# Kernel optimization log

Hardware: AMD Instinct MI355X
Metric: run time of the kernel (lower is better)

Reference implementation:

```python
import jax, jax.numpy as jnp
import numpy as np

NUM_CLASSES = 10
OUT_DIM = 16
NUM_ROUTING = 3
ROUTING_BIAS = 0.1


def _squash(s):
    # s: [B, C, D]; norm over last (out_capsule) dim, matches torch norm(dim=2)
    norm = jnp.linalg.norm(s, axis=2, keepdims=True)
    # s / (1+norm^2) / norm * norm^2 == s * norm / (1 + norm^2)
    return s * norm / (1.0 + norm * norm)


def setup_inputs() -> dict:
    key = jax.random.key(0)
    k1, k2 = jax.random.split(key)
    B, N, IN_DIM = 256, 2304, 8
    x = jax.random.normal(k1, (B, N, IN_DIM), dtype=jnp.float32)
    # kaiming-normal-ish init for W [N, in_dim, classes*out_dim]
    W = jax.random.normal(k2, (N, IN_DIM, NUM_CLASSES * OUT_DIM), dtype=jnp.float32) * np.sqrt(2.0 / IN_DIM)
    return {"x": x, "W": W}


def reference(x, W):
    B, N, _ = x.shape
    # broadcast-multiply+sum in original == per-capsule matmul
    u_hat = jnp.einsum('bni,nio->bno', x, W).reshape(B, N, NUM_CLASSES, OUT_DIM)
    u_hat_sg = jax.lax.stop_gradient(u_hat)
    b = jnp.zeros((B, N, NUM_CLASSES), dtype=x.dtype)
    v = None
    for i in range(NUM_ROUTING):
        c = jax.nn.softmax(b, axis=2)  # [B, N, C]
        if i == NUM_ROUTING - 1:
            s = jnp.einsum('bnc,bncd->bcd', c, u_hat) + ROUTING_BIAS
            v = _squash(s)
        else:
            s = jnp.einsum('bnc,bncd->bcd', c, u_hat_sg) + ROUTING_BIAS
            # NOTE: original updates b with pre-squash s (not v) -- kept faithful
            b = b + jnp.einsum('bncd,bcd->bnc', u_hat_sg, s)
    return v
```

## Files before the change

### kernel.cpp

```cpp
#include <hip/hip_runtime.h>
#include <math.h>

#define B_TOT   256
#define N_TOT   2304
#define IN_DIM  8
#define NC      10
#define OD      16
#define CD      160
#define RBIAS   0.1f

#define BTILE    64
#define NS       192
#define NPB      (N_TOT / NS)
#define NTHREADS 640
#define XR       (NPB * IN_DIM + 4)
#define LB       72
#define NF4      (B_TOT * CD / 4)
#define RCOLS    32
#define RGRPS    8
#define RYPER    (NS / RGRPS)

template <int FIRST>
__global__ __launch_bounds__(NTHREADS) void routing_round(
    const float* __restrict__ x,
    const float* __restrict__ W,
    const float* __restrict__ S_acc,
    float* __restrict__ part)
{
    __shared__ float sh_x[BTILE * XR];
    __shared__ float sh_lg[2][NC * LB];

    const int tid = threadIdx.x;
    const int b0  = blockIdx.x * BTILE;
    const int n0  = blockIdx.y * NPB;
    const int b   = tid & 63;
    const int cu  = __builtin_amdgcn_readfirstlane(tid >> 6);

    {
        const int XT4 = BTILE * (NPB * IN_DIM / 4);
        for (int k = tid; k < XT4; k += NTHREADS) {
            int bb   = k / (NPB * 2);
            int off4 = k - bb * (NPB * 2);
            float4 v = *(const float4*)(x + ((size_t)(b0 + bb) * N_TOT + n0) * IN_DIM + off4 * 4);
            *(float4*)(&sh_x[bb * XR + off4 * 4]) = v;
        }
    }

    float S[OD];
    if (!FIRST) {
        const float4* sp = (const float4*)(S_acc + (size_t)(b0 + b) * CD + cu * OD);
        #pragma unroll
        for (int q = 0; q < 4; q++) ((float4*)S)[q] = sp[q];
    }

    float acc[OD];
    #pragma unroll
    for (int d = 0; d < OD; d++) acc[d] = 0.f;

    __syncthreads();

    const float* Wc = W + cu * OD;

    for (int nn = 0; nn < NPB; nn++) {
        float xf[IN_DIM];
        {
            const float4* xp = (const float4*)(&sh_x[b * XR + nn * IN_DIM]);
            ((float4*)xf)[0] = xp[0];
            ((float4*)xf)[1] = xp[1];
        }

        const float* Wn = Wc + (size_t)(n0 + nn) * (IN_DIM * CD);
        float u[OD];
        #pragma unroll
        for (int d = 0; d < OD; d++) u[d] = xf[0] * Wn[d];
        #pragma unroll
        for (int i = 1; i < IN_DIM; i++) {
            const float* Wi = Wn + i * CD;
            #pragma unroll
            for (int d = 0; d < OD; d++) u[d] = fmaf(xf[i], Wi[d], u[d]);
        }

        if (!FIRST) {
            const int cur = nn & 1;
            float lg = 0.f;
            #pragma unroll
            for (int d = 0; d < OD; d++) lg = fmaf(u[d], S[d], lg);
            sh_lg[cur][cu * LB + b] = lg;
            __syncthreads();

            float m = -1e30f;
            float row[NC];
            #pragma unroll
            for (int k = 0; k < NC; k++) {
                row[k] = sh_lg[cur][k * LB + b];
                m = fmaxf(m, row[k]);
            }
            float den = 0.f;
            #pragma unroll
            for (int k = 0; k < NC; k++) den += __expf(row[k] - m);
            float cw = __expf(lg - m) / den;

            #pragma unroll
            for (int d = 0; d < OD; d++) acc[d] = fmaf(cw, u[d], acc[d]);
        } else {
            #pragma unroll
            for (int d = 0; d < OD; d++) acc[d] += u[d];
        }
    }

    float* dst = part + ((size_t)blockIdx.y * B_TOT + (b0 + b)) * CD + cu * OD;
    #pragma unroll
    for (int q = 0; q < 4; q++)
        ((float4*)dst)[q] = ((float4*)acc)[q];
}

__global__ __launch_bounds__(256) void reduce_round(
    const float* __restrict__ part,
    float* __restrict__ S_acc,
    float* __restrict__ v_out,
    float scale, int round)
{
    __shared__ float4 sh[RGRPS][RCOLS];

    const int col = threadIdx.x & (RCOLS - 1);
    const int grp = threadIdx.x >> 5;
    const int g   = blockIdx.x * RCOLS + col;

    const float4* p4 = (const float4*)part + (size_t)grp * NF4 + g;
    float4 s = { 0.f, 0.f, 0.f, 0.f };
    #pragma unroll 4
    for (int y = 0; y < RYPER; y++) {
        float4 t = p4[(size_t)y * RGRPS * NF4];
        s.x += t.x; s.y += t.y; s.z += t.z; s.w += t.w;
    }
    sh[grp][col] = s;
    __syncthreads();

    if (threadIdx.x < RCOLS) {
        float4 t = { 0.f, 0.f, 0.f, 0.f };
        #pragma unroll
        for (int k = 0; k < RGRPS; k++) {
            float4 q = sh[k][col];
            t.x += q.x; t.y += q.y; t.z += q.z; t.w += q.w;
        }
        t.x = t.x * scale + RBIAS;
        t.y = t.y * scale + RBIAS;
        t.z = t.z * scale + RBIAS;
        t.w = t.w * scale + RBIAS;

        if (round == 0) {
            ((float4*)S_acc)[g] = t;
        } else if (round == 1) {
            float4 o = ((float4*)S_acc)[g];
            o.x += t.x; o.y += t.y; o.z += t.z; o.w += t.w;
            ((float4*)S_acc)[g] = o;
        } else {
            float ss = t.x * t.x + t.y * t.y + t.z * t.z + t.w * t.w;
            ss += __shfl_xor(ss, 1, 64);
            ss += __shfl_xor(ss, 2, 64);
            float norm = sqrtf(ss);
            float k2 = norm / (1.0f + ss);
            float4 v = { t.x * k2, t.y * k2, t.z * k2, t.w * k2 };
            ((float4*)v_out)[g] = v;
        }
    }
}

extern "C" void kernel_launch(void* const* d_in, const int* in_sizes, int n_in,
                              void* d_out, int out_size, void* d_ws, size_t ws_size,
                              hipStream_t stream) {
    const float* x = (const float*)d_in[0];
    const float* W = (const float*)d_in[1];
    float* out = (float*)d_out;

    float* part  = (float*)d_ws;
    float* S_acc = part + (size_t)NS * B_TOT * CD;

    const dim3 rgrid(B_TOT / BTILE, NS);
    const int  RG = NF4 / RCOLS;

    routing_round<1><<<rgrid, NTHREADS, 0, stream>>>(x, W, S_acc, part);
    reduce_round<<<RG, 256, 0, stream>>>(part, S_acc, out, 0.1f, 0);

    routing_round<0><<<rgrid, NTHREADS, 0, stream>>>(x, W, S_acc, part);
    reduce_round<<<RG, 256, 0, stream>>>(part, S_acc, out, 1.0f, 1);

    routing_round<0><<<rgrid, NTHREADS, 0, stream>>>(x, W, S_acc, part);
    reduce_round<<<RG, 256, 0, stream>>>(part, S_acc, out, 1.0f, 2);
}
```

Baseline: 212.4 us.

## Cache u_hat in fp16 workspace for later routing rounds instead of recomputing

The first routing pass now also writes the per-capsule prediction vectors u_hat to workspace in half precision. The two later routing passes read them back instead of recomputing x·W. A software-prefetch of the next capsule's data is added in the cached kernel. The path runs only when the workspace is large enough, and otherwise falls back to recomputation. This trades compute for a large extra memory stream and adds fp16 rounding error to the logits and the final output.

```diff
diff --git a/kernel.cpp b/kernel.cpp
--- a/kernel.cpp
+++ b/kernel.cpp
@@ -1,4 +1,5 @@
 #include <hip/hip_runtime.h>
+#include <hip/hip_fp16.h>
 #include <math.h>
 
 #define B_TOT   256
@@ -20,15 +21,14 @@
 #define RGRPS    8
 #define RYPER    (NS / RGRPS)
 
-template <int FIRST>
-__global__ __launch_bounds__(NTHREADS) void routing_round(
+template <int STORE>
+__global__ __launch_bounds__(NTHREADS) void routing_r0(
     const float* __restrict__ x,
     const float* __restrict__ W,
-    const float* __restrict__ S_acc,
-    float* __restrict__ part)
+    float* __restrict__ part,
+    __half* __restrict__ uh)
 {
     __shared__ float sh_x[BTILE * XR];
-    __shared__ float sh_lg[2][NC * LB];
 
     const int tid = threadIdx.x;
     const int b0  = blockIdx.x * BTILE;
@@ -46,13 +46,6 @@
         }
     }
 
-    float S[OD];
-    if (!FIRST) {
-        const float4* sp = (const float4*)(S_acc + (size_t)(b0 + b) * CD + cu * OD);
-        #pragma unroll
-        for (int q = 0; q < 4; q++) ((float4*)S)[q] = sp[q];
-    }
-
     float acc[OD];
     #pragma unroll
     for (int d = 0; d < OD; d++) acc[d] = 0.f;
@@ -80,31 +73,17 @@
             for (int d = 0; d < OD; d++) u[d] = fmaf(xf[i], Wi[d], u[d]);
         }
 
-        if (!FIRST) {
-            const int cur = nn & 1;
-            float lg = 0.f;
+        #pragma unroll
+        for (int d = 0; d < OD; d++) acc[d] += u[d];
+
+        if (STORE) {
+            __half2 hp[8];
             #pragma unroll
-            for (int d = 0; d < OD; d++) lg = fmaf(u[d], S[d], lg);
-            sh_lg[cur][cu * LB + b] = lg;
-            __syncthreads();
-
-            float m = -1e30f;
-            float row[NC];
-            #pragma unroll
-            for (int k = 0; k < NC; k++) {
-                row[k] = sh_lg[cur][k * LB + b];
-                m = fmaxf(m, row[k]);
-            }
-            float den = 0.f;
-            #pragma unroll
-            for (int k = 0; k < NC; k++) den += __expf(row[k] - m);
-            float cw = __expf(lg - m) / den;
-
-            #pragma unroll
-            for (int d = 0; d < OD; d++) acc[d] = fmaf(cw, u[d], acc[d]);
-        } else {
-            #pragma unroll
-            for (int d = 0; d < OD; d++) acc[d] += u[d];
+            for (int q = 0; q < 8; q++)
+                hp[q] = __floats2half2_rn(u[2 * q], u[2 * q + 1]);
+            uint4* dst = (uint4*)(uh + ((size_t)((n0 + nn) * NC + cu) * B_TOT + (b0 + b)) * OD);
+            dst[0] = *(uint4*)&hp[0];
+            dst[1] = *(uint4*)&hp[4];
         }
     }
 
@@ -114,11 +93,165 @@
         ((float4*)dst)[q] = ((float4*)acc)[q];
 }
 
+__global__ __launch_bounds__(NTHREADS) void routing_cached(
+    const __half* __restrict__ uh,
+    const float* __restrict__ S_acc,
+    float* __restrict__ part)
+{
+    __shared__ float sh_lg[2][NC * LB];
+
+    const int tid = threadIdx.x;
+    const int b0  = blockIdx.x * BTILE;
+    const int n0  = blockIdx.y * NPB;
+    const int b   = tid & 63;
+    const int cu  = __builtin_amdgcn_readfirstlane(tid >> 6);
+
+    float S[OD];
+    {
+        const float4* sp = (const float4*)(S_acc + (size_t)(b0 + b) * CD + cu * OD);
+        #pragma unroll
+        for (int q = 0; q < 4; q++) ((float4*)S)[q] = sp[q];
+    }
+
+    float acc[OD];
+    #pragma unroll
+    for (int d = 0; d < OD; d++) acc[d] = 0.f;
+
+    const uint4* ub = (const uint4*)(uh + ((size_t)(n0 * NC + cu) * B_TOT + (b0 + b)) * OD);
+    const size_t nstride = (size_t)NC * B_TOT * 2;
+
+    uint4 p0 = ub[0], p1 = ub[1];
+
+    for (int nn = 0; nn < NPB; nn++) {
+        uint4 q0, q1;
+        if (nn + 1 < NPB) {
+            const uint4* nx = ub + (size_t)(nn + 1) * nstride;
+            q0 = nx[0]; q1 = nx[1];
+        }
+
+        float u[OD];
+        #pragma unroll
+        for (int j = 0; j < 4; j++) {
+            float2 f = __half22float2(((const __half2*)&p0)[j]);
+            u[2 * j] = f.x;  u[2 * j + 1] = f.y;
+        }
+        #pragma unroll
+        for (int j = 0; j < 4; j++) {
+            float2 f = __half22float2(((const __half2*)&p1)[j]);
+            u[8 + 2 * j] = f.x;  u[8 + 2 * j + 1] = f.y;
+        }
+
+        const int cur = nn & 1;
+        float lg = 0.f;
+        #pragma unroll
+        for (int d = 0; d < OD; d++) lg = fmaf(u[d], S[d], lg);
+        sh_lg[cur][cu * LB + b] = lg;
+        __syncthreads();
+
+        float m = -1e30f, row[NC];
+        #pragma unroll
+        for (int k = 0; k < NC; k++) {
+            row[k] = sh_lg[cur][k * LB + b];
+            m = fmaxf(m, row[k]);
+        }
+        float den = 0.f;
+        #pragma unroll
+        for (int k = 0; k < NC; k++) den += __expf(row[k] - m);
+        float cw = __expf(lg - m) / den;
+
+        #pragma unroll
+        for (int d = 0; d < OD; d++) acc[d] = fmaf(cw, u[d], acc[d]);
+
+        p0 = q0;  p1 = q1;
+    }
+
+    float* dst = part + ((size_t)blockIdx.y * B_TOT + (b0 + b)) * CD + cu * OD;
+    #pragma unroll
+    for (int q = 0; q < 4; q++)
+        ((float4*)dst)[q] = ((float4*)acc)[q];
+}
+
+__global__ __launch_bounds__(NTHREADS) void routing_scalar(
+    const float* __restrict__ x, const float* __restrict__ W,
+    const float* __restrict__ S_acc, float* __restrict__ part)
+{
+    __shared__ float sh_x[BTILE * XR];
+    __shared__ float sh_lg[2][NC * LB];
+
+    const int tid = threadIdx.x;
+    const int b0  = blockIdx.x * BTILE;
+    const int n0  = blockIdx.y * NPB;
+    const int b   = tid & 63;
+    const int cu  = __builtin_amdgcn_readfirstlane(tid >> 6);
+
+    {
+        const int XT4 = BTILE * (NPB * IN_DIM / 4);
+        for (int k = tid; k < XT4; k += NTHREADS) {
+            int bb   = k / (NPB * 2);
+            int off4 = k - bb * (NPB * 2);
+            float4 v = *(const float4*)(x + ((size_t)(b0 + bb) * N_TOT + n0) * IN_DIM + off4 * 4);
+            *(float4*)(&sh_x[bb * XR + off4 * 4]) = v;
+        }
+    }
+
+    float S[OD];
+    {
+        const float4* sp = (const float4*)(S_acc + (size_t)(b0 + b) * CD + cu * OD);
+        #pragma unroll
+        for (int q = 0; q < 4; q++) ((float4*)S)[q] = sp[q];
+    }
+
+    float acc[OD];
+    #pragma unroll
+    for (int d = 0; d < OD; d++) acc[d] = 0.f;
+
+    __syncthreads();
+
+    const float* Wc = W + cu * OD;
+
+    for (int nn = 0; nn < NPB; nn++) {
+        float xf[IN_DIM];
+        {
+            const float4* xp = (const float4*)(&sh_x[b * XR + nn * IN_DIM]);
+            ((float4*)xf)[0] = xp[0];
+            ((float4*)xf)[1] = xp[1];
+        }
+        const float* Wn = Wc + (size_t)(n0 + nn) * (IN_DIM * CD);
+        float u[OD];
+        #pragma unroll
+        for (int d = 0; d < OD; d++) u[d] = xf[0] * Wn[d];
+        #pragma unroll
+        for (int i = 1; i < IN_DIM; i++) {
+            const float* Wi = Wn + i * CD;
+            #pragma unroll
+            for (int d = 0; d < OD; d++) u[d] = fmaf(xf[i], Wi[d], u[d]);
+        }
+        const int cur = nn & 1;
+        float lg = 0.f;
+        #pragma unroll
+        for (int d = 0; d < OD; d++) lg = fmaf(u[d], S[d], lg);
+        sh_lg[cur][cu * LB + b] = lg;
+        __syncthreads();
+        float m = -1e30f, row[NC];
+        #pragma unroll
+        for (int k = 0; k < NC; k++) { row[k] = sh_lg[cur][k * LB + b]; m = fmaxf(m, row[k]); }
+        float den = 0.f;
+        #pragma unroll
+        for (int k = 0; k < NC; k++) den += __expf(row[k] - m);
+        float cw = __expf(lg - m) / den;
+        #pragma unroll
+        for (int d = 0; d < OD; d++) acc[d] = fmaf(cw, u[d], acc[d]);
+    }
+
+    float* dst = part + ((size_t)blockIdx.y * B_TOT + (b0 + b)) * CD + cu * OD;
+    #pragma unroll
+    for (int q = 0; q < 4; q++)
+        ((float4*)dst)[q] = ((float4*)acc)[q];
+}
+
 __global__ __launch_bounds__(256) void reduce_round(
-    const float* __restrict__ part,
-    float* __restrict__ S_acc,
-    float* __restrict__ v_out,
-    float scale, int round)
+    const float* __restrict__ part, float* __restrict__ S_acc,
+    float* __restrict__ v_out, float scale, int round)
 {
     __shared__ float4 sh[RGRPS][RCOLS];
 
@@ -175,16 +308,28 @@
 
     float* part  = (float*)d_ws;
     float* S_acc = part + (size_t)NS * B_TOT * CD;
+    __half* uh   = (__half*)(S_acc + (size_t)B_TOT * CD);
+
+    const size_t need = ((size_t)(NS + 1) * B_TOT * CD) * sizeof(float)
+                      + (size_t)N_TOT * NC * B_TOT * OD * sizeof(__half);
+    const bool cached = (ws_size >= need);
 
     const dim3 rgrid(B_TOT / BTILE, NS);
     const int  RG = NF4 / RCOLS;
 
-    routing_round<1><<<rgrid, NTHREADS, 0, stream>>>(x, W, S_acc, part);
-    reduce_round<<<RG, 256, 0, stream>>>(part, S_acc, out, 0.1f, 0);
-
-    routing_round<0><<<rgrid, NTHREADS, 0, stream>>>(x, W, S_acc, part);
-    reduce_round<<<RG, 256, 0, stream>>>(part, S_acc, out, 1.0f, 1);
-
-    routing_round<0><<<rgrid, NTHREADS, 0, stream>>>(x, W, S_acc, part);
-    reduce_round<<<RG, 256, 0, stream>>>(part, S_acc, out, 1.0f, 2);
-}
+    if (cached) {
+        routing_r0<1><<<rgrid, NTHREADS, 0, stream>>>(x, W, part, uh);
+        reduce_round<<<RG, 256, 0, stream>>>(part, S_acc, out, 0.1f, 0);
+        routing_cached<<<rgrid, NTHREADS, 0, stream>>>(uh, S_acc, part);
+        reduce_round<<<RG, 256, 0, stream>>>(part, S_acc, out, 1.0f, 1);
+        routing_cached<<<rgrid, NTHREADS, 0, stream>>>(uh, S_acc, part);
+        reduce_round<<<RG, 256, 0, stream>>>(part, S_acc, out, 1.0f, 2);
+    } else {
+        routing_r0<0><<<rgrid, NTHREADS, 0, stream>>>(x, W, part, nullptr);
+        reduce_round<<<RG, 256, 0, stream>>>(part, S_acc, out, 0.1f, 0);
+        routing_scalar<<<rgrid, NTHREADS, 0, stream>>>(x, W, S_acc, part);
+        reduce_round<<<RG, 256, 0, stream>>>(part, S_acc, out, 1.0f, 1);
+        routing_scalar<<<rgrid, NTHREADS, 0, stream>>>(x, W, S_acc, part);
+        reduce_round<<<RG, 256, 0, stream>>>(part, S_acc, out, 1.0f, 2);
+    }
+}
```

After: 237.4 us. 11.8% more time.
